# Kernel optimization log

Hardware: AMD Instinct MI355X
Metric: run time of the kernel (lower is better)

The kernel has to match this reference:

```python
import jax, jax.numpy as jnp
import numpy as np

DIM = 1024
NUM_HEADS = 16
HEAD_DIM = DIM // NUM_HEADS
SCALE = HEAD_DIM ** -0.5


def setup_inputs() -> dict:
    key = jax.random.key(0)
    ks = jax.random.split(key, 8)
    B, N, L = 2, 256, 8192
    x = jax.random.normal(ks[0], (B, N, DIM), dtype=jnp.float32)
    past_k = jax.random.normal(ks[1], (B, NUM_HEADS, L, HEAD_DIM), dtype=jnp.float32)
    past_v = jax.random.normal(ks[2], (B, NUM_HEADS, L, HEAD_DIM), dtype=jnp.float32)
    s = DIM ** -0.5
    w_qkv = jax.random.normal(ks[3], (DIM, 3 * DIM), dtype=jnp.float32) * s
    b_qkv = jnp.zeros((3 * DIM,), dtype=jnp.float32)
    w_proj = jax.random.normal(ks[4], (DIM, DIM), dtype=jnp.float32) * s
    b_proj = jnp.zeros((DIM,), dtype=jnp.float32)
    return {"x": x, "past_k": past_k, "past_v": past_v,
            "w_qkv": w_qkv, "b_qkv": b_qkv, "w_proj": w_proj, "b_proj": b_proj}


def reference(x, past_k, past_v, w_qkv, b_qkv, w_proj, b_proj):
    B, N, C = x.shape
    qkv = (x @ w_qkv + b_qkv).reshape(B, N, 3, NUM_HEADS, HEAD_DIM)
    qkv = jnp.transpose(qkv, (2, 0, 3, 1, 4))
    q, k_new, v_new = qkv[0], qkv[1], qkv[2]
    # Streaming KV cache append (torch.cat along seq dim)
    k_all = jnp.concatenate([past_k, k_new], axis=-2)  # [B, H, L+N, D]
    v_all = jnp.concatenate([past_v, v_new], axis=-2)
    # Scaled dot-product attention (non-causal full attention over cache)
    scores = jnp.einsum("bhnd,bhld->bhnl", q, k_all) * SCALE
    attn = jax.nn.softmax(scores, axis=-1)
    out = jnp.einsum("bhnl,bhld->bhnd", attn, v_all)  # [B, H, N, D]
    out = jnp.transpose(out, (0, 2, 1, 3)).reshape(B, N, C)
    return out @ w_proj + b_proj
```

## Files before the change

### kernel.cpp

```cpp
#include <hip/hip_runtime.h>
#include <hip/hip_bf16.h>


#define BB 2
#define NH 16
#define NQ 256
#define HD 64
#define DIMC 1024
#define LPAST 8192
#define TOTK 8448
#define NSPLIT 16

typedef __attribute__((ext_vector_type(8))) short short8;
typedef __attribute__((ext_vector_type(4))) float f32x4;
typedef __attribute__((ext_vector_type(16))) float f32x16;
typedef __attribute__((ext_vector_type(4))) int int4v;

#define DEVI static __device__ __forceinline__

DEVI float exp2g(float x) { return __builtin_amdgcn_exp2f(x); }

DEVI int cvtpk(float lo, float hi) {
  int r;
  asm("v_cvt_pk_bf16_f32 %0, %1, %2" : "=v"(r) : "v"(lo), "v"(hi));
  return r;
}
DEVI short f2bf(float f) {
  union { float f; unsigned u; } v; v.f = f;
  unsigned r = v.u + 0x7FFFu + ((v.u >> 16) & 1u);
  return (short)(r >> 16);
}
DEVI void ldsbar() {
  asm volatile("s_waitcnt lgkmcnt(0)" ::: "memory");
  __builtin_amdgcn_s_barrier();
}

template<int MODE>
__global__ __launch_bounds__(256, 2) void gemm_k(
    const float* __restrict__ A, const float* __restrict__ Bm,
    const float* __restrict__ bias, float* __restrict__ Cout,
    short* __restrict__ qbuf, float* __restrict__ knew, float* __restrict__ vnew,
    int M, int Nn, int K)
{
  __shared__ alignas(16) short As[64][72];
  __shared__ alignas(16) short Bs[64][72];
  const int tid = threadIdx.x;
  const int lane = tid & 63, wave = tid >> 6;
  const int nblk = Nn >> 6;
  const int bi = blockIdx.x / nblk, bj = blockIdx.x % nblk;
  const int wm = wave >> 1, wn = wave & 1;
  const int g = lane >> 4, l16 = lane & 15;
  f32x4 acc[2][2] = {};
  const int r = tid >> 2, q4 = (tid & 3) << 4;

  for (int k0 = 0; k0 < K; k0 += 64) {
    const float* pa = A + (size_t)(bi * 64 + r) * K + (k0 + q4);
    float4 a0 = ((const float4*)pa)[0];
    float4 a1 = ((const float4*)pa)[1];
    float4 a2 = ((const float4*)pa)[2];
    float4 a3 = ((const float4*)pa)[3];
    const float* pb = Bm + (size_t)(k0 + r) * Nn + (bj * 64 + q4);
    float4 b0 = ((const float4*)pb)[0];
    float4 b1 = ((const float4*)pb)[1];
    float4 b2 = ((const float4*)pb)[2];
    float4 b3 = ((const float4*)pb)[3];
    ldsbar();
    {
      int4v p0 = {cvtpk(a0.x,a0.y), cvtpk(a0.z,a0.w), cvtpk(a1.x,a1.y), cvtpk(a1.z,a1.w)};
      int4v p1 = {cvtpk(a2.x,a2.y), cvtpk(a2.z,a2.w), cvtpk(a3.x,a3.y), cvtpk(a3.z,a3.w)};
      *(int4v*)&As[r][q4]     = p0;
      *(int4v*)&As[r][q4 + 8] = p1;
    }
    Bs[q4+ 0][r] = f2bf(b0.x); Bs[q4+ 1][r] = f2bf(b0.y);
    Bs[q4+ 2][r] = f2bf(b0.z); Bs[q4+ 3][r] = f2bf(b0.w);
    Bs[q4+ 4][r] = f2bf(b1.x); Bs[q4+ 5][r] = f2bf(b1.y);
    Bs[q4+ 6][r] = f2bf(b1.z); Bs[q4+ 7][r] = f2bf(b1.w);
    Bs[q4+ 8][r] = f2bf(b2.x); Bs[q4+ 9][r] = f2bf(b2.y);
    Bs[q4+10][r] = f2bf(b2.z); Bs[q4+11][r] = f2bf(b2.w);
    Bs[q4+12][r] = f2bf(b3.x); Bs[q4+13][r] = f2bf(b3.y);
    Bs[q4+14][r] = f2bf(b3.z); Bs[q4+15][r] = f2bf(b3.w);
    ldsbar();
    #pragma unroll
    for (int kf = 0; kf < 2; ++kf) {
      short8 af[2], bfv[2];
      #pragma unroll
      for (int mt = 0; mt < 2; ++mt)
        af[mt] = *(const short8*)&As[wm*32 + mt*16 + l16][kf*32 + g*8];
      #pragma unroll
      for (int nt = 0; nt < 2; ++nt)
        bfv[nt] = *(const short8*)&Bs[wn*32 + nt*16 + l16][kf*32 + g*8];
      #pragma unroll
      for (int mt = 0; mt < 2; ++mt)
        #pragma unroll
        for (int nt = 0; nt < 2; ++nt)
          acc[mt][nt] = __builtin_amdgcn_mfma_f32_16x16x32_bf16(
              af[mt], bfv[nt], acc[mt][nt], 0, 0, 0);
    }
  }

  #pragma unroll
  for (int mt = 0; mt < 2; ++mt)
    #pragma unroll
    for (int nt = 0; nt < 2; ++nt)
      #pragma unroll
      for (int rg = 0; rg < 4; ++rg) {
        int row = bi*64 + wm*32 + mt*16 + g*4 + rg;
        int col = bj*64 + wn*32 + nt*16 + l16;
        float val = acc[mt][nt][rg] + bias[col];
        if (MODE == 0) {
          Cout[(size_t)row * Nn + col] = val;
        } else {
          int which = col >> 10, cc = col & 1023;
          int h = cc >> 6, d = cc & 63;
          int b = row >> 8, n = row & 255;
          size_t idx = (((size_t)(b*NH + h))*NQ + n)*HD + d;
          if (which == 0)      qbuf[idx] = f2bf(val * 0.180336878f);
          else if (which == 1) knew[idx] = val;
          else                 vnew[idx] = val;
        }
      }
}

__global__ __launch_bounds__(512, 2) void attn_k(
    const short* __restrict__ qbuf, const float* __restrict__ pastk,
    const float* __restrict__ pastv, const float* __restrict__ knew,
    const float* __restrict__ vnew, float* __restrict__ opart,
    float* __restrict__ mbuf, float* __restrict__ lbuf)
{
  __shared__ alignas(16) short Kt[2][64][64];
  __shared__ alignas(16) short Vt[2][64][64];
  const int tid = threadIdx.x;
  const int lane = tid & 63, wave = tid >> 6;
  const int h = lane >> 5, c = lane & 31;
  const int s = blockIdx.x & (NSPLIT - 1), bh = blockIdx.x / NSPLIT;
  const int kr = tid >> 3, kc8 = (tid & 7) << 3;
  const int vp = tid >> 4, vd4 = (tid & 15) << 2;
  const int vpi = ((vp>>4)<<5) | (((vp>>2)&1)<<4) | (((vp>>1)&1)<<3)
                | (((vp>>3)&1)<<2) | ((vp&1)<<1);
  const int csw = (c & 7) << 3;

  short8 qf[4];
  #pragma unroll
  for (int dk = 0; dk < 4; ++dk)
    qf[dk] = *(const short8*)(qbuf + ((size_t)bh*NQ + wave*32 + c)*HD + 16*dk + 8*h);

  f32x16 acc[2] = {};
  float m_s = -INFINITY, l_s = 0.f;

  const int first  = 8*s + (s < 4 ? s : 4);
  const int nsteps = 8 + (s < 4 ? 1 : 0);

  float kfl[8];
  float4 vA, vB;
  auto load = [&](int step) {
    const float* kp = (step < 128)
        ? pastk + ((size_t)bh*LPAST + step*64 + kr)*HD + kc8
        : knew  + ((size_t)bh*NQ + (step - 128)*64 + kr)*HD + kc8;
    *(float4*)&kfl[0] = *(const float4*)kp;
    *(float4*)&kfl[4] = *(const float4*)(kp + 4);
    const float* vq = (step < 128)
        ? pastv + ((size_t)bh*LPAST + step*64 + 2*vp)*HD + vd4
        : vnew  + ((size_t)bh*NQ + (step - 128)*64 + 2*vp)*HD + vd4;
    vA = *(const float4*)vq;
    vB = *(const float4*)(vq + HD);
  };
  auto stage = [&](int b) {
    int4v kp4 = {cvtpk(kfl[0],kfl[1]), cvtpk(kfl[2],kfl[3]),
                 cvtpk(kfl[4],kfl[5]), cvtpk(kfl[6],kfl[7])};
    *(int4v*)&Kt[b][kr][kc8 ^ ((kr & 7) << 3)] = kp4;
    const float* af = (const float*)&vA;
    const float* cf = (const float*)&vB;
    #pragma unroll
    for (int i = 0; i < 4; ++i) {
      int row = vd4 + i;
      *(int*)&Vt[b][row][vpi ^ ((row & 7) << 3)] = cvtpk(af[i], cf[i]);
    }
  };

  load(first);
  stage(0);
  if (nsteps > 1) load(first + 1);
  ldsbar();

  for (int it = 0; it < nsteps; ++it) {
    const int cur = it & 1;

    f32x16 sv0 = {}, sv1 = {};
    __builtin_amdgcn_s_setprio(1);
    #pragma unroll
    for (int dk = 0; dk < 4; ++dk) {
      short8 k0 = *(const short8*)&Kt[cur][c][(16*dk + 8*h) ^ csw];
      sv0 = __builtin_amdgcn_mfma_f32_32x32x16_bf16(k0, qf[dk], sv0, 0,0,0);
    }
    #pragma unroll
    for (int dk = 0; dk < 4; ++dk) {
      short8 k1 = *(const short8*)&Kt[cur][32 + c][(16*dk + 8*h) ^ csw];
      sv1 = __builtin_amdgcn_mfma_f32_32x32x16_bf16(k1, qf[dk], sv1, 0,0,0);
    }
    __builtin_amdgcn_s_setprio(0);

    if (it + 1 < nsteps) {
      stage(1 - cur);
      if (it + 2 < nsteps) load(first + it + 2);
    }

    float t16[16];
    #pragma unroll
    for (int r = 0; r < 16; ++r) t16[r] = fmaxf(sv0[r], sv1[r]);
    #pragma unroll
    for (int w = 8; w >= 1; w >>= 1)
      #pragma unroll
      for (int r = 0; r < w; ++r) t16[r] = fmaxf(t16[r], t16[r + w]);
    float mxh = t16[0];

    if (!__all(mxh <= m_s + 8.f)) {
      float mx = fmaxf(mxh, __shfl_xor(mxh, 32));
      float mn = fmaxf(m_s, mx);
      float al = exp2g(m_s - mn);
      l_s *= al;
      #pragma unroll
      for (int r = 0; r < 16; ++r) {
        float a = __shfl(al, (r&3) + 8*(r>>2) + 4*h);
        acc[0][r] *= a; acc[1][r] *= a;
      }
      m_s = mn;
    }
    float ss = 0.f;
    #pragma unroll
    for (int r = 0; r < 16; ++r) {
      float p0 = exp2g(sv0[r] - m_s); sv0[r] = p0;
      float p1 = exp2g(sv1[r] - m_s); sv1[r] = p1;
      ss += p0 + p1;
    }
    l_s += ss;

    short8 pa[4];
    #pragma unroll
    for (int kc = 0; kc < 4; ++kc) {
      int4v w;
      #pragma unroll
      for (int jd = 0; jd < 4; ++jd) {
        int r0 = 8*(jd>>1) + 4*(kc&1) + 2*(jd&1);
        w[jd] = (kc < 2) ? cvtpk(sv0[r0], sv0[r0+1])
                         : cvtpk(sv1[r0], sv1[r0+1]);
      }
      pa[kc] = __builtin_bit_cast(short8, w);
    }

    __builtin_amdgcn_s_setprio(1);
    #pragma unroll
    for (int kc = 0; kc < 4; ++kc) {
      #pragma unroll
      for (int dt = 0; dt < 2; ++dt) {
        short8 vf = *(const short8*)&Vt[cur][32*dt + c][(16*kc + 8*h) ^ csw];
        acc[dt] = __builtin_amdgcn_mfma_f32_32x32x16_bf16(pa[kc], vf, acc[dt], 0,0,0);
      }
    }
    __builtin_amdgcn_s_setprio(0);

    if (it + 1 < nsteps) ldsbar();
  }

  float l_tot = l_s + __shfl_xor(l_s, 32);
  size_t pbase = ((size_t)(bh * NSPLIT + s)) * NQ;
  #pragma unroll
  for (int dt = 0; dt < 2; ++dt)
    #pragma unroll
    for (int r = 0; r < 16; ++r) {
      int row = wave*32 + (r&3) + 8*(r>>2) + 4*h;
      opart[(pbase + row)*HD + 32*dt + c] = acc[dt][r];
    }
  if (lane < 32) {
    mbuf[pbase + wave*32 + c] = m_s;
    lbuf[pbase + wave*32 + c] = l_tot;
  }
}

__global__ __launch_bounds__(256) void combine_k(
    const float* __restrict__ opart, const float* __restrict__ mbuf,
    const float* __restrict__ lbuf, float* __restrict__ attnout)
{
  const int lane = threadIdx.x & 63, wave = threadIdx.x >> 6;
  const int rid = blockIdx.x * 4 + wave;
  const int bh = rid >> 8, n = rid & 255;
  const int b = bh >> 4, h = bh & 15;
  float M = -INFINITY;
  float ms[NSPLIT], ls[NSPLIT];
  #pragma unroll
  for (int s = 0; s < NSPLIT; ++s) {
    size_t base = ((size_t)(bh * NSPLIT + s)) * NQ + n;
    ms[s] = mbuf[base]; ls[s] = lbuf[base];
    M = fmaxf(M, ms[s]);
  }
  float denom = 0.f, o = 0.f;
  #pragma unroll
  for (int s = 0; s < NSPLIT; ++s) {
    float w = exp2g(ms[s] - M);
    denom += w * ls[s];
    o += w * opart[(((size_t)(bh * NSPLIT + s)) * NQ + n) * HD + lane];
  }
  attnout[((size_t)(b * NQ + n)) * DIMC + h * HD + lane] = o / denom;
}

extern "C" void kernel_launch(void* const* d_in, const int* in_sizes, int n_in,
                              void* d_out, int out_size, void* d_ws, size_t ws_size,
                              hipStream_t stream)
{
  const float* x     = (const float*)d_in[0];
  const float* pastk = (const float*)d_in[1];
  const float* pastv = (const float*)d_in[2];
  const float* wqkv  = (const float*)d_in[3];
  const float* bqkv  = (const float*)d_in[4];
  const float* wproj = (const float*)d_in[5];
  const float* bproj = (const float*)d_in[6];
  float* out = (float*)d_out;
  char* ws = (char*)d_ws;

  size_t off = 0;
  short* qbuf   = (short*)(ws + off); off += (size_t)BB*NH*NQ*HD*2;
  float* knew   = (float*)(ws + off); off += (size_t)BB*NH*NQ*HD*4;
  float* vnew   = (float*)(ws + off); off += (size_t)BB*NH*NQ*HD*4;
  float* opart  = (float*)(ws + off); off += (size_t)BB*NH*NSPLIT*NQ*HD*4;
  float* mbuf   = (float*)(ws + off); off += (size_t)BB*NH*NSPLIT*NQ*4;
  float* lbuf   = (float*)(ws + off); off += (size_t)BB*NH*NSPLIT*NQ*4;
  float* attnout= (float*)(ws + off); off += (size_t)BB*NQ*DIMC*4;

  gemm_k<1><<<(512/64)*(3072/64), 256, 0, stream>>>(
      x, wqkv, bqkv, nullptr, qbuf, knew, vnew, 512, 3072, 1024);
  attn_k<<<BB*NH*NSPLIT, 512, 0, stream>>>(
      qbuf, pastk, pastv, knew, vnew, opart, mbuf, lbuf);
  combine_k<<<BB*NH*NQ/4, 256, 0, stream>>>(opart, mbuf, lbuf, attnout);
  gemm_k<0><<<(512/64)*(1024/64), 256, 0, stream>>>(
      attnout, wproj, bproj, out, nullptr, nullptr, nullptr, 512, 1024, 1024);
}
```

Measured before the change: 90.33 us.

## Process two 32-row query tiles per wave in attention, halving block threads

The attention kernel now runs 4 waves of 256 threads instead of 8, with each wave handling 64 query rows as two 32-row tiles that share every K and V fragment read from LDS. This halves LDS fragment reads per MFMA and doubles per-thread staging work; global loads for V become strided scalar loads. It raises register pressure (two accumulator sets and four score tiles) and halves the waves available per block to hide latency.

```diff
diff --git a/kernel.cpp b/kernel.cpp
--- a/kernel.cpp
+++ b/kernel.cpp
@@ -121,7 +121,7 @@
       }
 }
 
-__global__ __launch_bounds__(512, 2) void attn_k(
+__global__ __launch_bounds__(256, 2) void attn_k(
     const short* __restrict__ qbuf, const float* __restrict__ pastk,
     const float* __restrict__ pastv, const float* __restrict__ knew,
     const float* __restrict__ vnew, float* __restrict__ opart,
@@ -130,51 +130,54 @@
   __shared__ alignas(16) short Kt[2][64][64];
   __shared__ alignas(16) short Vt[2][64][64];
   const int tid = threadIdx.x;
-  const int lane = tid & 63, wave = tid >> 6;
+  const int lane = tid & 63, qg = tid >> 6;
   const int h = lane >> 5, c = lane & 31;
   const int s = blockIdx.x & (NSPLIT - 1), bh = blockIdx.x / NSPLIT;
-  const int kr = tid >> 3, kc8 = (tid & 7) << 3;
-  const int vp = tid >> 4, vd4 = (tid & 15) << 2;
+  const int kr = tid >> 2, kd16 = (tid & 3) << 4;
+  const int vp = tid >> 3, vd = tid & 7;
   const int vpi = ((vp>>4)<<5) | (((vp>>2)&1)<<4) | (((vp>>1)&1)<<3)
                 | (((vp>>3)&1)<<2) | ((vp&1)<<1);
+  const int vswz = vpi ^ (vd << 3);
   const int csw = (c & 7) << 3;
 
-  short8 qf[4];
-  #pragma unroll
-  for (int dk = 0; dk < 4; ++dk)
-    qf[dk] = *(const short8*)(qbuf + ((size_t)bh*NQ + wave*32 + c)*HD + 16*dk + 8*h);
-
-  f32x16 acc[2] = {};
-  float m_s = -INFINITY, l_s = 0.f;
+  short8 qfA[4], qfB[4];
+  #pragma unroll
+  for (int dk = 0; dk < 4; ++dk) {
+    qfA[dk] = *(const short8*)(qbuf + ((size_t)bh*NQ + qg*64 + c)*HD + 16*dk + 8*h);
+    qfB[dk] = *(const short8*)(qbuf + ((size_t)bh*NQ + qg*64 + 32 + c)*HD + 16*dk + 8*h);
+  }
+
+  f32x16 accA[2] = {}, accB[2] = {};
+  float mA = -INFINITY, lA = 0.f, mB = -INFINITY, lB = 0.f;
 
   const int first  = 8*s + (s < 4 ? s : 4);
   const int nsteps = 8 + (s < 4 ? 1 : 0);
 
-  float kfl[8];
-  float4 vA, vB;
+  float kst[16], vlo[8], vhi[8];
   auto load = [&](int step) {
     const float* kp = (step < 128)
-        ? pastk + ((size_t)bh*LPAST + step*64 + kr)*HD + kc8
-        : knew  + ((size_t)bh*NQ + (step - 128)*64 + kr)*HD + kc8;
-    *(float4*)&kfl[0] = *(const float4*)kp;
-    *(float4*)&kfl[4] = *(const float4*)(kp + 4);
+        ? pastk + ((size_t)bh*LPAST + step*64 + kr)*HD + kd16
+        : knew  + ((size_t)bh*NQ + (step - 128)*64 + kr)*HD + kd16;
+    *(float4*)&kst[0]  = ((const float4*)kp)[0];
+    *(float4*)&kst[4]  = ((const float4*)kp)[1];
+    *(float4*)&kst[8]  = ((const float4*)kp)[2];
+    *(float4*)&kst[12] = ((const float4*)kp)[3];
     const float* vq = (step < 128)
-        ? pastv + ((size_t)bh*LPAST + step*64 + 2*vp)*HD + vd4
-        : vnew  + ((size_t)bh*NQ + (step - 128)*64 + 2*vp)*HD + vd4;
-    vA = *(const float4*)vq;
-    vB = *(const float4*)(vq + HD);
+        ? pastv + ((size_t)bh*LPAST + step*64 + 2*vp)*HD + vd
+        : vnew  + ((size_t)bh*NQ + (step - 128)*64 + 2*vp)*HD + vd;
+    #pragma unroll
+    for (int j = 0; j < 8; ++j) { vlo[j] = vq[8*j]; vhi[j] = vq[HD + 8*j]; }
   };
   auto stage = [&](int b) {
-    int4v kp4 = {cvtpk(kfl[0],kfl[1]), cvtpk(kfl[2],kfl[3]),
-                 cvtpk(kfl[4],kfl[5]), cvtpk(kfl[6],kfl[7])};
-    *(int4v*)&Kt[b][kr][kc8 ^ ((kr & 7) << 3)] = kp4;
-    const float* af = (const float*)&vA;
-    const float* cf = (const float*)&vB;
-    #pragma unroll
-    for (int i = 0; i < 4; ++i) {
-      int row = vd4 + i;
-      *(int*)&Vt[b][row][vpi ^ ((row & 7) << 3)] = cvtpk(af[i], cf[i]);
-    }
+    int4v k0 = {cvtpk(kst[0],kst[1]),  cvtpk(kst[2],kst[3]),
+                cvtpk(kst[4],kst[5]),  cvtpk(kst[6],kst[7])};
+    int4v k1 = {cvtpk(kst[8],kst[9]),  cvtpk(kst[10],kst[11]),
+                cvtpk(kst[12],kst[13]), cvtpk(kst[14],kst[15])};
+    *(int4v*)&Kt[b][kr][kd16 ^ ((kr & 7) << 3)]       = k0;
+    *(int4v*)&Kt[b][kr][(kd16 + 8) ^ ((kr & 7) << 3)] = k1;
+    #pragma unroll
+    for (int j = 0; j < 8; ++j)
+      *(int*)&Vt[b][vd + 8*j][vswz] = cvtpk(vlo[j], vhi[j]);
   };
 
   load(first);
@@ -185,17 +188,19 @@
   for (int it = 0; it < nsteps; ++it) {
     const int cur = it & 1;
 
-    f32x16 sv0 = {}, sv1 = {};
+    f32x16 svA0 = {}, svA1 = {}, svB0 = {}, svB1 = {};
     __builtin_amdgcn_s_setprio(1);
     #pragma unroll
     for (int dk = 0; dk < 4; ++dk) {
       short8 k0 = *(const short8*)&Kt[cur][c][(16*dk + 8*h) ^ csw];
-      sv0 = __builtin_amdgcn_mfma_f32_32x32x16_bf16(k0, qf[dk], sv0, 0,0,0);
+      svA0 = __builtin_amdgcn_mfma_f32_32x32x16_bf16(k0, qfA[dk], svA0, 0,0,0);
+      svB0 = __builtin_amdgcn_mfma_f32_32x32x16_bf16(k0, qfB[dk], svB0, 0,0,0);
     }
     #pragma unroll
     for (int dk = 0; dk < 4; ++dk) {
       short8 k1 = *(const short8*)&Kt[cur][32 + c][(16*dk + 8*h) ^ csw];
-      sv1 = __builtin_amdgcn_mfma_f32_32x32x16_bf16(k1, qf[dk], sv1, 0,0,0);
+      svA1 = __builtin_amdgcn_mfma_f32_32x32x16_bf16(k1, qfA[dk], svA1, 0,0,0);
+      svB1 = __builtin_amdgcn_mfma_f32_32x32x16_bf16(k1, qfB[dk], svB1, 0,0,0);
     }
     __builtin_amdgcn_s_setprio(0);
 
@@ -204,47 +209,86 @@
       if (it + 2 < nsteps) load(first + it + 2);
     }
 
-    float t16[16];
-    #pragma unroll
-    for (int r = 0; r < 16; ++r) t16[r] = fmaxf(sv0[r], sv1[r]);
-    #pragma unroll
-    for (int w = 8; w >= 1; w >>= 1)
-      #pragma unroll
-      for (int r = 0; r < w; ++r) t16[r] = fmaxf(t16[r], t16[r + w]);
-    float mxh = t16[0];
-
-    if (!__all(mxh <= m_s + 8.f)) {
-      float mx = fmaxf(mxh, __shfl_xor(mxh, 32));
-      float mn = fmaxf(m_s, mx);
-      float al = exp2g(m_s - mn);
-      l_s *= al;
+    short8 paA[4], paB[4];
+    {
+      float t16[16];
+      #pragma unroll
+      for (int r = 0; r < 16; ++r) t16[r] = fmaxf(svA0[r], svA1[r]);
+      #pragma unroll
+      for (int w = 8; w >= 1; w >>= 1)
+        #pragma unroll
+        for (int r = 0; r < w; ++r) t16[r] = fmaxf(t16[r], t16[r + w]);
+      if (!__all(t16[0] <= mA + 8.f)) {
+        float mx = fmaxf(t16[0], __shfl_xor(t16[0], 32));
+        float mn = fmaxf(mA, mx);
+        float al = exp2g(mA - mn);
+        lA *= al;
+        #pragma unroll
+        for (int r = 0; r < 16; ++r) {
+          float a = __shfl(al, (r&3) + 8*(r>>2) + 4*h);
+          accA[0][r] *= a; accA[1][r] *= a;
+        }
+        mA = mn;
+      }
+      float ss = 0.f;
       #pragma unroll
       for (int r = 0; r < 16; ++r) {
-        float a = __shfl(al, (r&3) + 8*(r>>2) + 4*h);
-        acc[0][r] *= a; acc[1][r] *= a;
-      }
-      m_s = mn;
-    }
-    float ss = 0.f;
-    #pragma unroll
-    for (int r = 0; r < 16; ++r) {
-      float p0 = exp2g(sv0[r] - m_s); sv0[r] = p0;
-      float p1 = exp2g(sv1[r] - m_s); sv1[r] = p1;
-      ss += p0 + p1;
-    }
-    l_s += ss;
-
-    short8 pa[4];
-    #pragma unroll
-    for (int kc = 0; kc < 4; ++kc) {
-      int4v w;
-      #pragma unroll
-      for (int jd = 0; jd < 4; ++jd) {
-        int r0 = 8*(jd>>1) + 4*(kc&1) + 2*(jd&1);
-        w[jd] = (kc < 2) ? cvtpk(sv0[r0], sv0[r0+1])
-                         : cvtpk(sv1[r0], sv1[r0+1]);
-      }
-      pa[kc] = __builtin_bit_cast(short8, w);
+        float p0 = exp2g(svA0[r] - mA); svA0[r] = p0;
+        float p1 = exp2g(svA1[r] - mA); svA1[r] = p1;
+        ss += p0 + p1;
+      }
+      lA += ss;
+      #pragma unroll
+      for (int kc = 0; kc < 4; ++kc) {
+        int4v w;
+        #pragma unroll
+        for (int jd = 0; jd < 4; ++jd) {
+          int r0 = 8*(jd>>1) + 4*(kc&1) + 2*(jd&1);
+          w[jd] = (kc < 2) ? cvtpk(svA0[r0], svA0[r0+1])
+                           : cvtpk(svA1[r0], svA1[r0+1]);
+        }
+        paA[kc] = __builtin_bit_cast(short8, w);
+      }
+    }
+    {
+      float t16[16];
+      #pragma unroll
+      for (int r = 0; r < 16; ++r) t16[r] = fmaxf(svB0[r], svB1[r]);
+      #pragma unroll
+      for (int w = 8; w >= 1; w >>= 1)
+        #pragma unroll
+        for (int r = 0; r < w; ++r) t16[r] = fmaxf(t16[r], t16[r + w]);
+      if (!__all(t16[0] <= mB + 8.f)) {
+        float mx = fmaxf(t16[0], __shfl_xor(t16[0], 32));
+        float mn = fmaxf(mB, mx);
+        float al = exp2g(mB - mn);
+        lB *= al;
+        #pragma unroll
+        for (int r = 0; r < 16; ++r) {
+          float a = __shfl(al, (r&3) + 8*(r>>2) + 4*h);
+          accB[0][r] *= a; accB[1][r] *= a;
+        }
+        mB = mn;
+      }
+      float ss = 0.f;
+      #pragma unroll
+      for (int r = 0; r < 16; ++r) {
+        float p0 = exp2g(svB0[r] - mB); svB0[r] = p0;
+        float p1 = exp2g(svB1[r] - mB); svB1[r] = p1;
+        ss += p0 + p1;
+      }
+      lB += ss;
+      #pragma unroll
+      for (int kc = 0; kc < 4; ++kc) {
+        int4v w;
+        #pragma unroll
+        for (int jd = 0; jd < 4; ++jd) {
+          int r0 = 8*(jd>>1) + 4*(kc&1) + 2*(jd&1);
+          w[jd] = (kc < 2) ? cvtpk(svB0[r0], svB0[r0+1])
+                           : cvtpk(svB1[r0], svB1[r0+1]);
+        }
+        paB[kc] = __builtin_bit_cast(short8, w);
+      }
     }
 
     __builtin_amdgcn_s_setprio(1);
@@ -253,7 +297,8 @@
       #pragma unroll
       for (int dt = 0; dt < 2; ++dt) {
         short8 vf = *(const short8*)&Vt[cur][32*dt + c][(16*kc + 8*h) ^ csw];
-        acc[dt] = __builtin_amdgcn_mfma_f32_32x32x16_bf16(pa[kc], vf, acc[dt], 0,0,0);
+        accA[dt] = __builtin_amdgcn_mfma_f32_32x32x16_bf16(paA[kc], vf, accA[dt], 0,0,0);
+        accB[dt] = __builtin_amdgcn_mfma_f32_32x32x16_bf16(paB[kc], vf, accB[dt], 0,0,0);
       }
     }
     __builtin_amdgcn_s_setprio(0);
@@ -261,18 +306,22 @@
     if (it + 1 < nsteps) ldsbar();
   }
 
-  float l_tot = l_s + __shfl_xor(l_s, 32);
+  float lAt = lA + __shfl_xor(lA, 32);
+  float lBt = lB + __shfl_xor(lB, 32);
   size_t pbase = ((size_t)(bh * NSPLIT + s)) * NQ;
   #pragma unroll
   for (int dt = 0; dt < 2; ++dt)
     #pragma unroll
     for (int r = 0; r < 16; ++r) {
-      int row = wave*32 + (r&3) + 8*(r>>2) + 4*h;
-      opart[(pbase + row)*HD + 32*dt + c] = acc[dt][r];
+      int rr = (r&3) + 8*(r>>2) + 4*h;
+      opart[(pbase + qg*64 + rr)*HD + 32*dt + c]      = accA[dt][r];
+      opart[(pbase + qg*64 + 32 + rr)*HD + 32*dt + c] = accB[dt][r];
     }
   if (lane < 32) {
-    mbuf[pbase + wave*32 + c] = m_s;
-    lbuf[pbase + wave*32 + c] = l_tot;
+    mbuf[pbase + qg*64 + c]      = mA;
+    lbuf[pbase + qg*64 + c]      = lAt;
+    mbuf[pbase + qg*64 + 32 + c] = mB;
+    lbuf[pbase + qg*64 + 32 + c] = lBt;
   }
 }
 
@@ -327,7 +376,7 @@
 
   gemm_k<1><<<(512/64)*(3072/64), 256, 0, stream>>>(
       x, wqkv, bqkv, nullptr, qbuf, knew, vnew, 512, 3072, 1024);
-  attn_k<<<BB*NH*NSPLIT, 512, 0, stream>>>(
+  attn_k<<<BB*NH*NSPLIT, 256, 0, stream>>>(
       qbuf, pastk, pastv, knew, vnew, opart, mbuf, lbuf);
   combine_k<<<BB*NH*NQ/4, 256, 0, stream>>>(opart, mbuf, lbuf, attnout);
   gemm_k<0><<<(512/64)*(1024/64), 256, 0, stream>>>(
```

Result: faster. 85.98 us (-4.8%).
